# Optimization experiments

Hardware: AMD Instinct MI355X
Metric: run time of the kernel (lower is better)

The kernel has to match this reference:

```python
import jax, jax.numpy as jnp
import numpy as np
from jax import lax

EPOCHS = 10  # self.epoch in the torch module


def setup_inputs() -> dict:
    key = jax.random.key(0)
    k1, k2 = jax.random.split(key)
    # (num_patches, groups, channels_per_group, kh, kw)
    patches = jax.random.normal(k1, (40000, 4, 16, 5, 5), dtype=jnp.float32)
    # torch: torch.randn([groups, K, D]) * 0.1
    centroids_init = jax.random.normal(k2, (4, 64, 400), dtype=jnp.float32) * 0.1
    return {"patches": patches, "centroids_init": centroids_init}


def reference(patches, centroids_init):
    N, G, C, H, W = patches.shape
    K = centroids_init.shape[1]
    D = C * H * W
    # [G, N, D] flattened patches per group
    pf = jnp.transpose(patches.reshape(N, G, D), (1, 0, 2))

    def step(centroids, _):
        # half squared norm of each centroid: [G, K]
        c2 = 0.5 * jnp.sum(centroids * centroids, axis=2)
        # scores[g,n,k] = <c_gk, p_gn> - 0.5||c_gk||^2  (max over k == nearest centroid)
        scores = jnp.einsum('gkd,gnd->gnk', centroids, pf) - c2[:, None, :]
        labels = jnp.argmax(scores, axis=2)                       # [G, N]
        S = jax.nn.one_hot(labels, K, dtype=pf.dtype)             # [G, N, K]
        summation = jnp.einsum('gnk,gnd->gkd', S, pf)             # [G, K, D]
        counts = jnp.sum(S, axis=1)                               # [G, K]
        new_c = summation / jnp.where(counts == 0, 1.0, counts)[:, :, None]
        # torch: centroids[:, where(counts==0)[1], :] = 0  -> zero that cluster
        # index across ALL groups if empty in any group
        bad = jnp.any(counts == 0, axis=0)                        # [K]
        new_c = jnp.where(bad[None, :, None], 0.0, new_c)
        return new_c, None

    centroids, _ = lax.scan(step, centroids_init, None, length=EPOCHS)
    # reshape to conv weight layout (out_channels, channels_per_group, kh, kw)
    return centroids.reshape(G * K, C, H, W)
```

## Files before the change

### kernel.cpp

```cpp
#include <hip/hip_runtime.h>

#define NPTS   40000
#define NG     4
#define NK     64
#define ND     400
#define NQ     100
#define PT     128
#define NCHUNK 25
#define NTILES 313
#define NSPL   16

typedef _Float16 f16x4 __attribute__((ext_vector_type(4)));
typedef float    f32x4 __attribute__((ext_vector_type(4)));

struct __align__(16) HL { f16x4 hi; f16x4 lo; };

__device__ __forceinline__ HL split4(float4 v) {
    float s0 = v.x * 64.0f, s1 = v.y * 64.0f, s2 = v.z * 64.0f, s3 = v.w * 64.0f;
    _Float16 a0 = (_Float16)s0, a1 = (_Float16)s1, a2 = (_Float16)s2, a3 = (_Float16)s3;
    HL h;
    h.hi = f16x4{a0, a1, a2, a3};
    h.lo = f16x4{(_Float16)(s0 - (float)a0), (_Float16)(s1 - (float)a1),
                 (_Float16)(s2 - (float)a2), (_Float16)(s3 - (float)a3)};
    return h;
}

__global__ __launch_bounds__(256)
void prepass_kernel(const float* __restrict__ patches, HL* __restrict__ ps)
{
    const int total = NPTS * NG * NQ;
    for (int i = blockIdx.x * 256 + threadIdx.x; i < total; i += gridDim.x * 256) {
        int n = i / (NG * NQ);
        int r = i - n * (NG * NQ);
        int g = r / NQ, q = r - g * NQ;
        ps[((size_t)g * NPTS + n) * NQ + q] = split4(((const float4*)patches)[i]);
    }
}

__global__ __launch_bounds__(128)
void centprep_kernel(const float* __restrict__ cent, HL* __restrict__ cs,
                     float* __restrict__ c2g)
{
    const int gk = blockIdx.x, t = threadIdx.x;
    __shared__ float p4[4];
    if (t < NQ) cs[(size_t)gk * NQ + t] = split4(((const float4*)cent)[gk * NQ + t]);
    if (t >= 100 && t < 104) {
        int j = t - 100;
        const float* c = cent + (size_t)gk * ND + 100 * j;
        float s = 0.0f;
        #pragma unroll
        for (int d = 0; d < 100; d += 4) {
            float4 v = *(const float4*)(c + d);
            s = fmaf(v.x, v.x, fmaf(v.y, v.y, fmaf(v.z, v.z, fmaf(v.w, v.w, s))));
        }
        p4[j] = s;
    }
    __syncthreads();
    if (t == 0) c2g[gk] = 2048.0f * (p4[0] + p4[1] + p4[2] + p4[3]);
}

__global__ __launch_bounds__(256)
void assign_kernel(const HL* __restrict__ ps,
                   const HL* __restrict__ cs,
                   const float* __restrict__ c2g,
                   int*   __restrict__ lr,
                   int*   __restrict__ pcnt)
{
    const int g    = blockIdx.y;
    const int tile = blockIdx.x;
    const int t    = threadIdx.x;
    const int n0   = tile * PT;

    __shared__ _Float16 A1[2][PT][20];
    __shared__ _Float16 A2[2][PT][20];
    __shared__ _Float16 B1[2][NK][20];
    __shared__ _Float16 B2[2][NK][20];
    __shared__ float c2s[NK];
    __shared__ int   cnt[NK];

    if (t < NK) { c2s[t] = c2g[g * NK + t]; cnt[t] = 0; }

    const int w   = t >> 6;
    const int l   = t & 63;
    const int q   = l >> 4;
    const int r15 = l & 15;

    const int rh = t & 127;
    const int hh = t >> 7;
    int nn = n0 + rh; if (nn >= NPTS) nn = NPTS - 1;
    const HL* prow = ps + ((size_t)g * NPTS + nn) * NQ;
    const HL* crow = cs + ((size_t)g * NK + (t >> 2)) * NQ;
    const int jj = t & 3;
    const int cc = t >> 2;

    f32x4 acc[2][4];
    {
        f32x4 z = {0.f, 0.f, 0.f, 0.f};
        #pragma unroll
        for (int i = 0; i < 2; ++i)
            #pragma unroll
            for (int j = 0; j < 4; ++j) acc[i][j] = z;
    }

    HL ha0 = prow[2 * hh];
    HL ha1 = prow[2 * hh + 1];
    HL hb  = crow[jj];
    *(f16x4*)&A1[0][rh][8 * hh]     = ha0.hi;
    *(f16x4*)&A2[0][rh][8 * hh]     = ha0.lo;
    *(f16x4*)&A1[0][rh][8 * hh + 4] = ha1.hi;
    *(f16x4*)&A2[0][rh][8 * hh + 4] = ha1.lo;
    *(f16x4*)&B1[0][cc][4 * jj]     = hb.hi;
    *(f16x4*)&B2[0][cc][4 * jj]     = hb.lo;
    __syncthreads();
    ha0 = prow[4 + 2 * hh];
    ha1 = prow[4 + 2 * hh + 1];
    hb  = crow[4 + jj];

    for (int c = 0; c < NCHUNK; ++c) {
        const int cur = c & 1;

        f16x4 a1v[2], a2v[2], b1v[4], b2v[4];
        #pragma unroll
        for (int pi = 0; pi < 2; ++pi) {
            int p = 32 * w + 16 * pi + r15;
            a1v[pi] = *(const f16x4*)&A1[cur][p][4 * q];
            a2v[pi] = *(const f16x4*)&A2[cur][p][4 * q];
        }
        #pragma unroll
        for (int cj = 0; cj < 4; ++cj) {
            int n = 16 * cj + r15;
            b1v[cj] = *(const f16x4*)&B1[cur][n][4 * q];
            b2v[cj] = *(const f16x4*)&B2[cur][n][4 * q];
        }
        #pragma unroll
        for (int pi = 0; pi < 2; ++pi)
            #pragma unroll
            for (int cj = 0; cj < 4; ++cj) {
                acc[pi][cj] = __builtin_amdgcn_mfma_f32_16x16x16f16(a2v[pi], b1v[cj], acc[pi][cj], 0, 0, 0);
                acc[pi][cj] = __builtin_amdgcn_mfma_f32_16x16x16f16(a1v[pi], b2v[cj], acc[pi][cj], 0, 0, 0);
                acc[pi][cj] = __builtin_amdgcn_mfma_f32_16x16x16f16(a1v[pi], b1v[cj], acc[pi][cj], 0, 0, 0);
            }

        if (c + 1 < NCHUNK) {
            const int nxt = cur ^ 1;
            *(f16x4*)&A1[nxt][rh][8 * hh]     = ha0.hi;
            *(f16x4*)&A2[nxt][rh][8 * hh]     = ha0.lo;
            *(f16x4*)&A1[nxt][rh][8 * hh + 4] = ha1.hi;
            *(f16x4*)&A2[nxt][rh][8 * hh + 4] = ha1.lo;
            *(f16x4*)&B1[nxt][cc][4 * jj]     = hb.hi;
            *(f16x4*)&B2[nxt][cc][4 * jj]     = hb.lo;
        }
        __syncthreads();
        if (c + 2 < NCHUNK) {
            const int q0 = 4 * (c + 2);
            ha0 = prow[q0 + 2 * hh];
            ha1 = prow[q0 + 2 * hh + 1];
            hb  = crow[q0 + jj];
        }
    }

    #pragma unroll
    for (int pi = 0; pi < 2; ++pi) {
        #pragma unroll
        for (int r = 0; r < 4; ++r) {
            float m  = acc[pi][0][r] - c2s[r15];
            int best = r15;
            #pragma unroll
            for (int cj = 1; cj < 4; ++cj) {
                int n = 16 * cj + r15;
                float s = acc[pi][cj][r] - c2s[n];
                if (s > m) { m = s; best = n; }
            }
            #pragma unroll
            for (int off = 1; off < 16; off <<= 1) {
                float om = __shfl_xor(m, off);
                int   ob = __shfl_xor(best, off);
                if (om > m || (om == m && ob < best)) { m = om; best = ob; }
            }
            if (r15 == 0) {
                int p  = 32 * w + 16 * pi + 4 * q + r;
                int np = n0 + p;
                if (np < NPTS) {
                    int rk = atomicAdd(&cnt[best], 1);
                    lr[(size_t)g * NPTS + np] = (rk << 8) | best;
                }
            }
        }
    }
    __syncthreads();
    if (t < NK) pcnt[((size_t)g * NTILES + tile) * NK + t] = cnt[t];
}

__global__ __launch_bounds__(256)
void scatter2_kernel(const int* __restrict__ lr,
                     const int* __restrict__ pcnt,
                     int* __restrict__ order,
                     int* __restrict__ cbase,
                     int* __restrict__ counts)
{
    const int tile = blockIdx.x, g = blockIdx.y, t = threadIdx.x;
    __shared__ unsigned short cnt_tk[NTILES * NK];
    __shared__ int part [4][NK];
    __shared__ int part2[4][NK];
    __shared__ int kbase[NK];
    __shared__ int tpre[NK];

    const int* pg = pcnt + (size_t)g * NTILES * NK;
    for (int i = t; i < NTILES * NK; i += 256)
        cnt_tk[i] = (unsigned short)pg[i];
    __syncthreads();

    {
        int k = t & 63, p = t >> 6;
        int s1 = 0, s2 = 0;
        for (int tl = p; tl < NTILES; tl += 4) {
            int v = cnt_tk[tl * NK + k];
            s1 += v;
            if (tl < tile) s2 += v;
        }
        part [p][k] = s1;
        part2[p][k] = s2;
    }
    __syncthreads();
    if (t < NK) {
        part[0][t] = part[0][t] + part[1][t] + part[2][t] + part[3][t];
        tpre[t]    = part2[0][t] + part2[1][t] + part2[2][t] + part2[3][t];
    }
    __syncthreads();
    if (t == 0) {
        int run = 0;
        for (int k = 0; k < NK; ++k) { kbase[k] = run; run += part[0][k]; }
    }
    __syncthreads();
    if (tile == 0 && t < NK) {
        cbase[g * NK + t]  = kbase[t];
        counts[g * NK + t] = part[0][t];
    }
    const int n = tile * PT + t;
    if (t < PT && n < NPTS) {
        int packed = lr[(size_t)g * NPTS + n];
        int L = packed & 63, r = packed >> 8;
        order[(size_t)g * NPTS + kbase[L] + tpre[L] + r] = n;
    }
}

__global__ __launch_bounds__(512, 2)
void gather_kernel(const HL*  __restrict__ ps,
                   const int* __restrict__ order,
                   const int* __restrict__ cbase,
                   const int* __restrict__ counts,
                   float* __restrict__ psum)
{
    const int s = blockIdx.x, k = blockIdx.y, g = blockIdx.z;
    const int t = threadIdx.x;
    const int base = cbase[g * NK + k];
    const int cnt  = counts[g * NK + k];
    const int start = base + (cnt * s) / NSPL;
    const int end   = base + (cnt * (s + 1)) / NSPL;

    const int slot = t / 100;
    const int q    = t - slot * 100;

    __shared__ float sums[5][ND];

    float4 acc = make_float4(0.f, 0.f, 0.f, 0.f);
    if (t < 500) {
        const int* ord = order + (size_t)g * NPTS;
        #pragma unroll 2
        for (int i = start + slot; i < end; i += 5) {
            int n = ord[i];
            HL h = ps[((size_t)g * NPTS + n) * NQ + q];
            acc.x += (float)h.hi[0] + (float)h.lo[0];
            acc.y += (float)h.hi[1] + (float)h.lo[1];
            acc.z += (float)h.hi[2] + (float)h.lo[2];
            acc.w += (float)h.hi[3] + (float)h.lo[3];
        }
        *(float4*)&sums[slot][4 * q] = acc;
    }
    __syncthreads();
    if (t < NQ) {
        float4 a0 = *(const float4*)&sums[0][4 * t];
        float4 a1 = *(const float4*)&sums[1][4 * t];
        float4 a2 = *(const float4*)&sums[2][4 * t];
        float4 a3 = *(const float4*)&sums[3][4 * t];
        float4 a4 = *(const float4*)&sums[4][4 * t];
        float4 o;
        o.x = a0.x + a1.x + a2.x + a3.x + a4.x;
        o.y = a0.y + a1.y + a2.y + a3.y + a4.y;
        o.z = a0.z + a1.z + a2.z + a3.z + a4.z;
        o.w = a0.w + a1.w + a2.w + a3.w + a4.w;
        float* dst = psum + (((size_t)(g * NK + k)) * NSPL + s) * ND + 4 * t;
        *(float4*)dst = o;
    }
}

__global__ __launch_bounds__(128)
void update_kernel(const float* __restrict__ psum,
                   const int*   __restrict__ counts,
                   float* __restrict__ outc,
                   HL*    __restrict__ cs,
                   float* __restrict__ c2g)
{
    const int gk = blockIdx.x;
    const int g = gk >> 6, k = gk & 63;
    const int t = threadIdx.x;

    __shared__ float qp[NQ];
    __shared__ float p4[4];

    const bool bad = (counts[0 * NK + k] == 0) | (counts[1 * NK + k] == 0) |
                     (counts[2 * NK + k] == 0) | (counts[3 * NK + k] == 0);
    const int  c  = counts[g * NK + k];
    const float inv = 1.0f / (float)(c == 0 ? 1 : c);

    if (t < NQ) {
        float4 s = make_float4(0.f, 0.f, 0.f, 0.f);
        const float* p = psum + ((size_t)gk * NSPL) * ND + 4 * t;
        #pragma unroll
        for (int sp = 0; sp < NSPL; ++sp) {
            float4 v = *(const float4*)(p + (size_t)sp * ND);
            s.x += v.x; s.y += v.y; s.z += v.z; s.w += v.w;
        }
        float4 c64;
        c64.x = bad ? 0.0f : s.x * inv;
        c64.y = bad ? 0.0f : s.y * inv;
        c64.z = bad ? 0.0f : s.z * inv;
        c64.w = bad ? 0.0f : s.w * inv;
        float4 o = make_float4(c64.x * 0.015625f, c64.y * 0.015625f,
                               c64.z * 0.015625f, c64.w * 0.015625f);
        *(float4*)(outc + (size_t)gk * ND + 4 * t) = o;
        _Float16 a0 = (_Float16)c64.x, a1 = (_Float16)c64.y,
                 a2 = (_Float16)c64.z, a3 = (_Float16)c64.w;
        HL h;
        h.hi = f16x4{a0, a1, a2, a3};
        h.lo = f16x4{(_Float16)(c64.x - (float)a0), (_Float16)(c64.y - (float)a1),
                     (_Float16)(c64.z - (float)a2), (_Float16)(c64.w - (float)a3)};
        cs[(size_t)gk * NQ + t] = h;
        qp[t] = fmaf(o.x, o.x, fmaf(o.y, o.y, fmaf(o.z, o.z, o.w * o.w)));
    }
    __syncthreads();
    if (t < 4) {
        float s = 0.0f;
        for (int i = 25 * t; i < 25 * t + 25; ++i) s += qp[i];
        p4[t] = s;
    }
    __syncthreads();
    if (t == 0) c2g[gk] = 2048.0f * (((p4[0] + p4[1]) + p4[2]) + p4[3]);
}

extern "C" void kernel_launch(void* const* d_in, const int* in_sizes, int n_in,
                              void* d_out, int out_size, void* d_ws, size_t ws_size,
                              hipStream_t stream)
{
    const float* patches = (const float*)d_in[0];
    const float* cinit   = (const float*)d_in[1];
    float* out = (float*)d_out;

    char* wp = (char*)d_ws;
    HL* PS = (HL*)wp;               wp += (size_t)NPTS * NG * NQ * sizeof(HL);
    HL* CS = (HL*)wp;               wp += (size_t)NG * NK * NQ * sizeof(HL);
    float* c2g = (float*)wp;        wp += (size_t)NG * NK * 4;
    float* centA = (float*)wp;      wp += (size_t)NG * NK * ND * 4;
    float* centB = (float*)wp;      wp += (size_t)NG * NK * ND * 4;
    int* lr      = (int*)wp;        wp += (size_t)NG * NPTS * 4;
    int* order   = (int*)wp;        wp += (size_t)NG * NPTS * 4;
    int* pcnt    = (int*)wp;        wp += (size_t)NG * NTILES * NK * 4;
    int* cbase   = (int*)wp;        wp += (size_t)NG * NK * 4;
    int* counts  = (int*)wp;        wp += (size_t)NG * NK * 4;
    float* psum  = (float*)wp;

    prepass_kernel<<<4096, 256, 0, stream>>>(patches, PS);
    centprep_kernel<<<NG * NK, 128, 0, stream>>>(cinit, CS, c2g);

    const float* cur = cinit;
    for (int e = 0; e < 10; ++e) {
        assign_kernel<<<dim3(NTILES, NG), 256, 0, stream>>>(PS, CS, c2g, lr, pcnt);
        scatter2_kernel<<<dim3(NTILES, NG), 256, 0, stream>>>(lr, pcnt, order, cbase, counts);
        gather_kernel<<<dim3(NSPL, NK, NG), 512, 0, stream>>>(PS, order, cbase, counts, psum);
        float* nxt = (e == 9) ? out : ((e & 1) ? centB : centA);
        update_kernel<<<NG * NK, 128, 0, stream>>>(psum, counts, nxt, CS, c2g);
        cur = nxt;
    }
    (void)cur;
}
```

Measured before the change: 1.663 ms.

## Double assign K-chunk depth and narrow label/count buffers to 16/8-bit

The assign kernel now stages 32 f16 elements per chunk instead of 16 (13 chunks instead of 25), with a padded shared-memory stride and zero-fill for the tail. This halves the number of barriers and global-load rounds per tile. Separately, per-point labels are stored as 16-bit and per-tile counts as 8-bit, which shrinks the traffic between assign and scatter. The scatter kernel loads those counts with 32-bit vector reads. The narrowing assumes per-tile counts stay below 256, which holds because each tile has 128 points.

```diff
diff --git a/kernel.cpp b/kernel.cpp
--- a/kernel.cpp
+++ b/kernel.cpp
@@ -6,9 +6,10 @@
 #define ND     400
 #define NQ     100
 #define PT     128
-#define NCHUNK 25
+#define NCHUNK 13
 #define NTILES 313
 #define NSPL   16
+#define LSTR   36
 
 typedef _Float16 f16x4 __attribute__((ext_vector_type(4)));
 typedef float    f32x4 __attribute__((ext_vector_type(4)));
@@ -22,6 +23,13 @@
     h.hi = f16x4{a0, a1, a2, a3};
     h.lo = f16x4{(_Float16)(s0 - (float)a0), (_Float16)(s1 - (float)a1),
                  (_Float16)(s2 - (float)a2), (_Float16)(s3 - (float)a3)};
+    return h;
+}
+
+__device__ __forceinline__ HL hlzero() {
+    HL h;
+    h.hi = f16x4{(_Float16)0.f, (_Float16)0.f, (_Float16)0.f, (_Float16)0.f};
+    h.lo = h.hi;
     return h;
 }
 
@@ -63,18 +71,18 @@
 void assign_kernel(const HL* __restrict__ ps,
                    const HL* __restrict__ cs,
                    const float* __restrict__ c2g,
-                   int*   __restrict__ lr,
-                   int*   __restrict__ pcnt)
+                   unsigned short* __restrict__ lr,
+                   unsigned char*  __restrict__ pcnt)
 {
     const int g    = blockIdx.y;
     const int tile = blockIdx.x;
     const int t    = threadIdx.x;
     const int n0   = tile * PT;
 
-    __shared__ _Float16 A1[2][PT][20];
-    __shared__ _Float16 A2[2][PT][20];
-    __shared__ _Float16 B1[2][NK][20];
-    __shared__ _Float16 B2[2][NK][20];
+    __shared__ _Float16 A1[2][PT][LSTR];
+    __shared__ _Float16 A2[2][PT][LSTR];
+    __shared__ _Float16 B1[2][NK][LSTR];
+    __shared__ _Float16 B2[2][NK][LSTR];
     __shared__ float c2s[NK];
     __shared__ int   cnt[NK];
 
@@ -102,60 +110,76 @@
             for (int j = 0; j < 4; ++j) acc[i][j] = z;
     }
 
-    HL ha0 = prow[2 * hh];
-    HL ha1 = prow[2 * hh + 1];
-    HL hb  = crow[jj];
-    *(f16x4*)&A1[0][rh][8 * hh]     = ha0.hi;
-    *(f16x4*)&A2[0][rh][8 * hh]     = ha0.lo;
-    *(f16x4*)&A1[0][rh][8 * hh + 4] = ha1.hi;
-    *(f16x4*)&A2[0][rh][8 * hh + 4] = ha1.lo;
-    *(f16x4*)&B1[0][cc][4 * jj]     = hb.hi;
-    *(f16x4*)&B2[0][cc][4 * jj]     = hb.lo;
-    __syncthreads();
-    ha0 = prow[4 + 2 * hh];
-    ha1 = prow[4 + 2 * hh + 1];
-    hb  = crow[4 + jj];
+    HL a[4], b[2];
+
+    #pragma unroll
+    for (int m = 0; m < 4; ++m) { int qa = 4 * hh + m; a[m] = (qa < NQ) ? prow[qa] : hlzero(); }
+    #pragma unroll
+    for (int m = 0; m < 2; ++m) { int qb = 2 * jj + m; b[m] = (qb < NQ) ? crow[qb] : hlzero(); }
+    #pragma unroll
+    for (int m = 0; m < 4; ++m) {
+        *(f16x4*)&A1[0][rh][4 * (4 * hh + m)] = a[m].hi;
+        *(f16x4*)&A2[0][rh][4 * (4 * hh + m)] = a[m].lo;
+    }
+    #pragma unroll
+    for (int m = 0; m < 2; ++m) {
+        *(f16x4*)&B1[0][cc][4 * (2 * jj + m)] = b[m].hi;
+        *(f16x4*)&B2[0][cc][4 * (2 * jj + m)] = b[m].lo;
+    }
+    __syncthreads();
+    #pragma unroll
+    for (int m = 0; m < 4; ++m) { int qa = 8 + 4 * hh + m; a[m] = (qa < NQ) ? prow[qa] : hlzero(); }
+    #pragma unroll
+    for (int m = 0; m < 2; ++m) { int qb = 8 + 2 * jj + m; b[m] = (qb < NQ) ? crow[qb] : hlzero(); }
 
     for (int c = 0; c < NCHUNK; ++c) {
         const int cur = c & 1;
 
-        f16x4 a1v[2], a2v[2], b1v[4], b2v[4];
         #pragma unroll
-        for (int pi = 0; pi < 2; ++pi) {
-            int p = 32 * w + 16 * pi + r15;
-            a1v[pi] = *(const f16x4*)&A1[cur][p][4 * q];
-            a2v[pi] = *(const f16x4*)&A2[cur][p][4 * q];
-        }
-        #pragma unroll
-        for (int cj = 0; cj < 4; ++cj) {
-            int n = 16 * cj + r15;
-            b1v[cj] = *(const f16x4*)&B1[cur][n][4 * q];
-            b2v[cj] = *(const f16x4*)&B2[cur][n][4 * q];
-        }
-        #pragma unroll
-        for (int pi = 0; pi < 2; ++pi)
+        for (int s = 0; s < 2; ++s) {
+            f16x4 a1v[2], a2v[2], b1v[4], b2v[4];
+            #pragma unroll
+            for (int pi = 0; pi < 2; ++pi) {
+                int p = 32 * w + 16 * pi + r15;
+                a1v[pi] = *(const f16x4*)&A1[cur][p][4 * (4 * s + q)];
+                a2v[pi] = *(const f16x4*)&A2[cur][p][4 * (4 * s + q)];
+            }
             #pragma unroll
             for (int cj = 0; cj < 4; ++cj) {
-                acc[pi][cj] = __builtin_amdgcn_mfma_f32_16x16x16f16(a2v[pi], b1v[cj], acc[pi][cj], 0, 0, 0);
-                acc[pi][cj] = __builtin_amdgcn_mfma_f32_16x16x16f16(a1v[pi], b2v[cj], acc[pi][cj], 0, 0, 0);
-                acc[pi][cj] = __builtin_amdgcn_mfma_f32_16x16x16f16(a1v[pi], b1v[cj], acc[pi][cj], 0, 0, 0);
-            }
+                int n = 16 * cj + r15;
+                b1v[cj] = *(const f16x4*)&B1[cur][n][4 * (4 * s + q)];
+                b2v[cj] = *(const f16x4*)&B2[cur][n][4 * (4 * s + q)];
+            }
+            #pragma unroll
+            for (int pi = 0; pi < 2; ++pi)
+                #pragma unroll
+                for (int cj = 0; cj < 4; ++cj) {
+                    acc[pi][cj] = __builtin_amdgcn_mfma_f32_16x16x16f16(a2v[pi], b1v[cj], acc[pi][cj], 0, 0, 0);
+                    acc[pi][cj] = __builtin_amdgcn_mfma_f32_16x16x16f16(a1v[pi], b2v[cj], acc[pi][cj], 0, 0, 0);
+                    acc[pi][cj] = __builtin_amdgcn_mfma_f32_16x16x16f16(a1v[pi], b1v[cj], acc[pi][cj], 0, 0, 0);
+                }
+        }
 
         if (c + 1 < NCHUNK) {
             const int nxt = cur ^ 1;
-            *(f16x4*)&A1[nxt][rh][8 * hh]     = ha0.hi;
-            *(f16x4*)&A2[nxt][rh][8 * hh]     = ha0.lo;
-            *(f16x4*)&A1[nxt][rh][8 * hh + 4] = ha1.hi;
-            *(f16x4*)&A2[nxt][rh][8 * hh + 4] = ha1.lo;
-            *(f16x4*)&B1[nxt][cc][4 * jj]     = hb.hi;
-            *(f16x4*)&B2[nxt][cc][4 * jj]     = hb.lo;
+            #pragma unroll
+            for (int m = 0; m < 4; ++m) {
+                *(f16x4*)&A1[nxt][rh][4 * (4 * hh + m)] = a[m].hi;
+                *(f16x4*)&A2[nxt][rh][4 * (4 * hh + m)] = a[m].lo;
+            }
+            #pragma unroll
+            for (int m = 0; m < 2; ++m) {
+                *(f16x4*)&B1[nxt][cc][4 * (2 * jj + m)] = b[m].hi;
+                *(f16x4*)&B2[nxt][cc][4 * (2 * jj + m)] = b[m].lo;
+            }
         }
         __syncthreads();
         if (c + 2 < NCHUNK) {
-            const int q0 = 4 * (c + 2);
-            ha0 = prow[q0 + 2 * hh];
-            ha1 = prow[q0 + 2 * hh + 1];
-            hb  = crow[q0 + jj];
+            const int q0 = 8 * (c + 2);
+            #pragma unroll
+            for (int m = 0; m < 4; ++m) { int qa = q0 + 4 * hh + m; a[m] = (qa < NQ) ? prow[qa] : hlzero(); }
+            #pragma unroll
+            for (int m = 0; m < 2; ++m) { int qb = q0 + 2 * jj + m; b[m] = (qb < NQ) ? crow[qb] : hlzero(); }
         }
     }
 
@@ -182,32 +206,32 @@
                 int np = n0 + p;
                 if (np < NPTS) {
                     int rk = atomicAdd(&cnt[best], 1);
-                    lr[(size_t)g * NPTS + np] = (rk << 8) | best;
+                    lr[(size_t)g * NPTS + np] = (unsigned short)((rk << 8) | best);
                 }
             }
         }
     }
     __syncthreads();
-    if (t < NK) pcnt[((size_t)g * NTILES + tile) * NK + t] = cnt[t];
+    if (t < NK) pcnt[((size_t)g * NTILES + tile) * NK + t] = (unsigned char)cnt[t];
 }
 
 __global__ __launch_bounds__(256)
-void scatter2_kernel(const int* __restrict__ lr,
-                     const int* __restrict__ pcnt,
+void scatter2_kernel(const unsigned short* __restrict__ lr,
+                     const unsigned char* __restrict__ pcnt,
                      int* __restrict__ order,
                      int* __restrict__ cbase,
                      int* __restrict__ counts)
 {
     const int tile = blockIdx.x, g = blockIdx.y, t = threadIdx.x;
-    __shared__ unsigned short cnt_tk[NTILES * NK];
+    __shared__ unsigned char cnt_tk[NTILES * NK];
     __shared__ int part [4][NK];
     __shared__ int part2[4][NK];
     __shared__ int kbase[NK];
     __shared__ int tpre[NK];
 
-    const int* pg = pcnt + (size_t)g * NTILES * NK;
-    for (int i = t; i < NTILES * NK; i += 256)
-        cnt_tk[i] = (unsigned short)pg[i];
+    const unsigned int* pg32 = (const unsigned int*)(pcnt + (size_t)g * NTILES * NK);
+    for (int i = t; i < NTILES * NK / 4; i += 256)
+        ((unsigned int*)cnt_tk)[i] = pg32[i];
     __syncthreads();
 
     {
@@ -357,29 +381,26 @@
     float* out = (float*)d_out;
 
     char* wp = (char*)d_ws;
-    HL* PS = (HL*)wp;               wp += (size_t)NPTS * NG * NQ * sizeof(HL);
-    HL* CS = (HL*)wp;               wp += (size_t)NG * NK * NQ * sizeof(HL);
-    float* c2g = (float*)wp;        wp += (size_t)NG * NK * 4;
-    float* centA = (float*)wp;      wp += (size_t)NG * NK * ND * 4;
-    float* centB = (float*)wp;      wp += (size_t)NG * NK * ND * 4;
-    int* lr      = (int*)wp;        wp += (size_t)NG * NPTS * 4;
-    int* order   = (int*)wp;        wp += (size_t)NG * NPTS * 4;
-    int* pcnt    = (int*)wp;        wp += (size_t)NG * NTILES * NK * 4;
-    int* cbase   = (int*)wp;        wp += (size_t)NG * NK * 4;
-    int* counts  = (int*)wp;        wp += (size_t)NG * NK * 4;
-    float* psum  = (float*)wp;
+    HL* PS = (HL*)wp;                wp += (size_t)NPTS * NG * NQ * sizeof(HL);
+    HL* CS = (HL*)wp;                wp += (size_t)NG * NK * NQ * sizeof(HL);
+    float* c2g = (float*)wp;         wp += (size_t)NG * NK * 4;
+    float* centA = (float*)wp;       wp += (size_t)NG * NK * ND * 4;
+    float* centB = (float*)wp;       wp += (size_t)NG * NK * ND * 4;
+    int* order   = (int*)wp;         wp += (size_t)NG * NPTS * 4;
+    int* cbase   = (int*)wp;         wp += (size_t)NG * NK * 4;
+    int* counts  = (int*)wp;         wp += (size_t)NG * NK * 4;
+    float* psum  = (float*)wp;       wp += (size_t)NG * NK * NSPL * ND * 4;
+    unsigned short* lr = (unsigned short*)wp;  wp += (size_t)NG * NPTS * 2;
+    unsigned char* pcnt = (unsigned char*)wp;
 
     prepass_kernel<<<4096, 256, 0, stream>>>(patches, PS);
     centprep_kernel<<<NG * NK, 128, 0, stream>>>(cinit, CS, c2g);
 
-    const float* cur = cinit;
     for (int e = 0; e < 10; ++e) {
         assign_kernel<<<dim3(NTILES, NG), 256, 0, stream>>>(PS, CS, c2g, lr, pcnt);
         scatter2_kernel<<<dim3(NTILES, NG), 256, 0, stream>>>(lr, pcnt, order, cbase, counts);
         gather_kernel<<<dim3(NSPL, NK, NG), 512, 0, stream>>>(PS, order, cbase, counts, psum);
         float* nxt = (e == 9) ? out : ((e & 1) ? centB : centA);
         update_kernel<<<NG * NK, 128, 0, stream>>>(psum, counts, nxt, CS, c2g);
-        cur = nxt;
-    }
-    (void)cur;
-}
+    }
+}
```

New measurement: 1.652 ms. Within noise of the previous version (-0.7%).
